# Performance work log

Measured on AMD Instinct MI355X. Metric: run time of the kernel, lower is better.

Reference implementation:

```python
import jax, jax.numpy as jnp
import numpy as np

KH, KW = 3, 3
STRIDE = (1, 1)
PAD = (1, 1)
DIL = (1, 1)

def _unfold(x, kh, kw, stride, padding, dilation):
    # Faithful torch.nn.functional.unfold: output (B, C*kh*kw, L) with
    # feature ordering channel-slowest, then kh, then kw.
    B, C, H, W = x.shape
    h_out = (H + 2 * padding[0] - dilation[0] * (kh - 1) - 1) // stride[0] + 1
    w_out = (W + 2 * padding[1] - dilation[1] * (kw - 1) - 1) // stride[1] + 1
    xp = jnp.pad(x, ((0, 0), (0, 0), (padding[0], padding[0]), (padding[1], padding[1])))
    rows = []
    for i in range(kh):  # small fixed kernel loop (9 slices), not a data-dim loop
        for j in range(kw):
            r0 = i * dilation[0]
            c0 = j * dilation[1]
            patch = xp[:, :, r0:r0 + h_out * stride[0]:stride[0],
                             c0:c0 + w_out * stride[1]:stride[1]]  # (B,C,h_out,w_out)
            rows.append(patch)
    # stack -> (B, C, kh*kw, h_out, w_out); reorder so feature dim = C*kh*kw
    p = jnp.stack(rows, axis=2)
    p = p.reshape(B, C * kh * kw, h_out * w_out)
    return p, h_out, w_out

def transform_transposed_unfolded_input(inp_unf):
    # Default hook: identity (as in the base class).
    return inp_unf

def reference(x, weight, bias):
    B = x.shape[0]
    O = weight.shape[0]
    inp_unf, h_out, w_out = _unfold(x, KH, KW, STRIDE, PAD, DIL)   # (B, C*k*k, L)
    inp_t = jnp.swapaxes(inp_unf, 1, 2)                            # (B, L, C*k*k)
    inp_t = transform_transposed_unfolded_input(inp_t)
    w2d = weight.reshape(O, -1)                                    # (O, C*k*k)
    out_unf = jnp.einsum('blk,ok->bol', inp_t, w2d)                # (B, O, L)
    out = out_unf.reshape(B, O, h_out, w_out)
    out = out + bias.reshape(1, O, 1, 1)
    return out

def setup_inputs() -> dict:
    key = jax.random.key(0)
    k1, k2, k3 = jax.random.split(key, 3)
    x = jax.random.normal(k1, (32, 128, 56, 56), dtype=jnp.float32)
    fan_in = 128 * KH * KW
    weight = jax.random.normal(k2, (256, 128, KH, KW), dtype=jnp.float32) / np.sqrt(fan_in)
    bias = jax.random.normal(k3, (256,), dtype=jnp.float32) * 0.01
    return {"x": x, "weight": weight, "bias": bias}
```

## Files before the change

### kernel.cpp

```cpp
#include <hip/hip_runtime.h>
#include <hip/hip_bf16.h>
#include <cstdint>

typedef float f32x4 __attribute__((ext_vector_type(4)));
typedef short bf16x8 __attribute__((ext_vector_type(8)));
typedef short short8 __attribute__((ext_vector_type(8)));

#define CIN   128
#define WIMG  56
#define HWSZ  3136
#define OCH   256
#define HP    58
#define WP    58

__global__ void small_prep(const float* __restrict__ wsrc,
                           __hip_bfloat16* __restrict__ wb,
                           __hip_bfloat16* __restrict__ xb) {
    int bidx = blockIdx.x;
    if (bidx < 456) {
        int idx = bidx * 256 + threadIdx.x;
        int c8  = idx & 15;
        int t   = idx >> 4;
        int b   = t / 228;
        int pos = t - b * 228;
        int h, w;
        if (pos < 58)       { h = 0;             w = pos; }
        else if (pos < 116) { h = 57;            w = pos - 58; }
        else if (pos < 172) { h = pos - 116 + 1; w = 0; }
        else                { h = pos - 172 + 1; w = 57; }
        uint4 z = {0, 0, 0, 0};
        *(uint4*)((char*)xb + (((size_t)(b * HP + h) * WP + w) * CIN + c8 * 8) * 2) = z;
    } else {
        int idx = (bidx - 456) * 256 + threadIdx.x;
        int c    = idx & 127;
        int rest = idx >> 7;
        int o    = rest & 255;
        int ij   = rest >> 8;
        wb[idx] = __float2bfloat16(wsrc[((size_t)o * CIN + c) * 9 + ij]);
    }
}

__global__ __launch_bounds__(256)
void cast_transpose_x(const float* __restrict__ x,
                      __hip_bfloat16* __restrict__ xb) {
    __shared__ float tile[64][33];
    const int hw0 = blockIdx.x * 32;
    const int c0  = blockIdx.y * 64;
    const int b   = blockIdx.z;

    const int lx = threadIdx.x & 31;
    const int lc = threadIdx.x >> 5;
    const float* src = x + ((size_t)(b * CIN + c0 + lc) * HWSZ) + hw0 + lx;
#pragma unroll
    for (int k = 0; k < 8; ++k)
        tile[lc + k * 8][lx] = src[(size_t)(k * 8) * HWSZ];
    __syncthreads();

    const int slot = threadIdx.x & 7;
    const int hwl  = threadIdx.x >> 3;
    int hw = hw0 + hwl;
    int h = hw / WIMG;
    int w = hw - h * WIMG;
    short8 v;
#pragma unroll
    for (int j = 0; j < 8; ++j) {
        __hip_bfloat16 hb = __float2bfloat16(tile[slot * 8 + j][hwl]);
        v[j] = *reinterpret_cast<short*>(&hb);
    }
    *(short8*)(xb + (((size_t)b * HP + (h + 1)) * WP + (w + 1)) * CIN + c0 + slot * 8) = v;
}

__device__ __forceinline__ void gload16(const void* g, void* l) {
    __builtin_amdgcn_global_load_lds(
        (const __attribute__((address_space(1))) unsigned*)g,
        (__attribute__((address_space(3))) unsigned*)l,
        16, 0, 0);
}

__global__ __launch_bounds__(512, 2)
void conv_gemm(const __hip_bfloat16* __restrict__ xb,
               const __hip_bfloat16* __restrict__ wb,
               const float* __restrict__ bias,
               float* __restrict__ out) {
    extern __shared__ __attribute__((aligned(16))) char smem[];

    const int tid = threadIdx.x;
    const int wv  = tid >> 6;
    const int ln  = tid & 63;

    int bid = blockIdx.x;
    bid = (bid & 7) * 49 + (bid >> 3);
    const int m0 = bid * 256;

    const int srow = tid >> 3;
    const int cs   = tid & 7;
    const int colsrc = ((cs * 16) ^ ((srow & 7) << 4)) >> 1;
    int aOff[4], bOff[4];
#pragma unroll
    for (int q = 0; q < 4; ++q) {
        int row = q * 64 + srow;
        int p  = m0 + row;
        int b  = p / HWSZ;
        int hw = p - b * HWSZ;
        int h  = hw / WIMG;
        int w  = hw - h * WIMG;
        aOff[q] = ((b * HP + h) * WP + w) * CIN + colsrc;
        bOff[q] = row * CIN + colsrc;
    }
    const int ldsd = tid * 16;

#define SA(buf,q,offA_) gload16(xb + aOff[q] + (offA_), smem + (buf)*65536 + (q)*8192 + ldsd)
#define SB(buf,q,offB_) gload16(wb + bOff[q] + (offB_), smem + (buf)*65536 + 32768 + (q)*8192 + ldsd)

    const int wm  = wv >> 2;
    const int wn  = wv & 3;
    const int fr  = ln & 15;
    const int kby = (ln >> 4) * 16;
    const int swz = (ln & 7) << 4;

    f32x4 acc[8][4] = {};
    bf16x8 af[4][2], bq0[2][2], bq1[2][2];

#define READ_A(base, mh) do {                                                 \
    _Pragma("unroll") for (int mi = 0; mi < 4; ++mi)                          \
    _Pragma("unroll") for (int kk = 0; kk < 2; ++kk)                          \
        af[mi][kk] = *(const bf16x8*)((base) +                                \
            (wm*128 + (mh)*64 + mi*16 + fr)*128 + ((kk*64 + kby) ^ swz));     \
} while (0)

#define READ_B(base, nh, dst) do {                                            \
    _Pragma("unroll") for (int ni = 0; ni < 2; ++ni)                          \
    _Pragma("unroll") for (int kk = 0; kk < 2; ++kk)                          \
        dst[ni][kk] = *(const bf16x8*)((base) + 32768 +                       \
            (wn*64 + (nh)*32 + ni*16 + fr)*128 + ((kk*64 + kby) ^ swz));      \
} while (0)

#define MQ(mh, nh, B) do {                                                    \
    _Pragma("unroll") for (int kk = 0; kk < 2; ++kk)                          \
    _Pragma("unroll") for (int mi = 0; mi < 4; ++mi)                          \
    _Pragma("unroll") for (int ni = 0; ni < 2; ++ni)                          \
        acc[(mh)*4+mi][(nh)*2+ni] = __builtin_amdgcn_mfma_f32_16x16x32_bf16(  \
            af[mi][kk], B[ni][kk], acc[(mh)*4+mi][(nh)*2+ni], 0, 0, 0);       \
} while (0)

#define VMW(N) do {                                                           \
    asm volatile("s_waitcnt vmcnt(" #N ")" ::: "memory");                     \
    __builtin_amdgcn_sched_barrier(0);                                        \
} while (0)

#define PHASE(MQCALL) do {                                                    \
    __builtin_amdgcn_s_barrier();                                             \
    asm volatile("s_waitcnt lgkmcnt(0)" ::: "memory");                        \
    __builtin_amdgcn_sched_barrier(0);                                        \
    __builtin_amdgcn_s_setprio(1);                                            \
    MQCALL;                                                                   \
    __builtin_amdgcn_s_setprio(0);                                            \
    __builtin_amdgcn_sched_barrier(0);                                        \
} while (0)

    const char* base0 = smem;
    const char* base1 = smem + 65536;

    SA(0,0,0); SA(0,2,0); SB(0,0,0); SB(0,1,0); SB(0,2,0); SB(0,3,0); SA(0,1,0); SA(0,3,0);
    SA(1,0,64); SA(1,2,64);
    asm volatile("s_waitcnt vmcnt(2)" ::: "memory");
    __builtin_amdgcn_s_barrier();

#pragma unroll 1
    for (int i = 0; i < 9; ++i) {
        const int iiA = i / 3,       jjA = i - 3 * iiA;
        const int iiB = (i + 1) / 3, jjB = (i + 1) - 3 * iiB;
        const int offA1 = (iiA * WP + jjA) * CIN + 64;
        const int offB1 = i * (OCH * CIN) + 64;
        const int offA2 = (iiB * WP + jjB) * CIN;
        const int offB2 = (i + 1) * (OCH * CIN);
        const int offA3 = offA2 + 64;
        const bool pf = (i < 8);

        READ_A(base0, 0);
        READ_B(base0, 0, bq0);
        SB(1,0,offB1); SB(1,1,offB1);
        PHASE(MQ(0, 0, bq0));
        __builtin_amdgcn_s_barrier();

        READ_B(base0, 1, bq1);
        SB(1,2,offB1); SB(1,3,offB1);
        PHASE(MQ(0, 1, bq1));
        VMW(6);
        __builtin_amdgcn_s_barrier();

        READ_A(base0, 1);
        SA(1,1,offA1); SA(1,3,offA1);
        PHASE(MQ(1, 1, bq1));
        __builtin_amdgcn_s_barrier();

        if (pf) { SA(0,0,offA2); SA(0,2,offA2); }
        PHASE(MQ(1, 0, bq0));
        if (pf) VMW(4); else VMW(2);
        __builtin_amdgcn_s_barrier();

        READ_A(base1, 0);
        READ_B(base1, 0, bq0);
        if (pf) { SB(0,0,offB2); SB(0,1,offB2); }
        PHASE(MQ(0, 0, bq0));
        __builtin_amdgcn_s_barrier();

        READ_B(base1, 1, bq1);
        if (pf) { SB(0,2,offB2); SB(0,3,offB2); }
        PHASE(MQ(0, 1, bq1));
        if (pf) VMW(6); else VMW(0);
        __builtin_amdgcn_s_barrier();

        READ_A(base1, 1);
        if (pf) { SA(0,1,offA2); SA(0,3,offA2); }
        PHASE(MQ(1, 1, bq1));
        __builtin_amdgcn_s_barrier();

        if (pf) { SA(1,0,offA3); SA(1,2,offA3); }
        PHASE(MQ(1, 0, bq0));
        if (pf) {
            VMW(4);
            __builtin_amdgcn_s_barrier();
        }
    }
#undef SA
#undef SB
#undef READ_A
#undef READ_B
#undef MQ
#undef PHASE
#undef VMW

    const int laneR4 = (ln >> 4) * 4;
    float bn[4];
#pragma unroll
    for (int ni = 0; ni < 4; ++ni)
        bn[ni] = bias[wn * 64 + ni * 16 + fr];

#pragma unroll
    for (int mi = 0; mi < 8; ++mi) {
        int p0 = m0 + wm * 128 + mi * 16 + laneR4;
        int b  = p0 / HWSZ;
        int hw = p0 - b * HWSZ;
#pragma unroll
        for (int ni = 0; ni < 4; ++ni) {
            int n = wn * 64 + ni * 16 + fr;
            float4 v;
            v.x = acc[mi][ni][0] + bn[ni];
            v.y = acc[mi][ni][1] + bn[ni];
            v.z = acc[mi][ni][2] + bn[ni];
            v.w = acc[mi][ni][3] + bn[ni];
            *(float4*)(out + ((size_t)(b * OCH + n) * HWSZ + hw)) = v;
        }
    }
}

extern "C" void kernel_launch(void* const* d_in, const int* in_sizes, int n_in,
                              void* d_out, int out_size, void* d_ws, size_t ws_size,
                              hipStream_t stream) {
    const float* x    = (const float*)d_in[0];
    const float* w    = (const float*)d_in[1];
    const float* bias = (const float*)d_in[2];
    float* out = (float*)d_out;

    char* ws = (char*)d_ws;
    __hip_bfloat16* xbuf = (__hip_bfloat16*)ws;
    __hip_bfloat16* wbuf = (__hip_bfloat16*)(ws + 27557888);

    hipFuncSetAttribute(reinterpret_cast<const void*>(conv_gemm),
                        hipFuncAttributeMaxDynamicSharedMemorySize, 131072);

    small_prep<<<1608, 256, 0, stream>>>(w, wbuf, xbuf);
    cast_transpose_x<<<dim3(98, 2, 32), dim3(256), 0, stream>>>(x, xbuf);
    conv_gemm<<<392, 512, 131072, stream>>>(xbuf, wbuf, bias, out);
}
```

Measured before the change: 100.5 us.

## Software-pipeline LDS fragment reads with double-buffered A/B registers in GEMM loop

Restructures the main K loop of the implicit-GEMM conv kernel so LDS-to-register fragment reads for the next MFMA quadrant are issued before and during the current quadrant's MFMAs. It uses separate A register sets (af0/af1) and even/odd B sets, with partial lgkmcnt waits replacing full waits. Global-to-LDS prefetch is regrouped so whole A+B half-tiles are issued together, and the prologue preloads the first fragments. This is meant to hide LDS read latency behind matrix math, at the cost of more VGPRs and a more delicate waitcnt and barrier ordering.

```diff
diff --git a/kernel.cpp b/kernel.cpp
--- a/kernel.cpp
+++ b/kernel.cpp
@@ -110,7 +110,7 @@
     const int ldsd = tid * 16;
 
 #define SA(buf,q,offA_) gload16(xb + aOff[q] + (offA_), smem + (buf)*65536 + (q)*8192 + ldsd)
-#define SB(buf,q,offB_) gload16(wb + bOff[q] + (offB_), smem + (buf)*65536 + 32768 + (q)*8192 + ldsd)
+#define SBW(buf,q,offB_) gload16(wb + bOff[q] + (offB_), smem + (buf)*65536 + 32768 + (q)*8192 + ldsd)
 
     const int wm  = wv >> 2;
     const int wn  = wv & 3;
@@ -119,117 +119,117 @@
     const int swz = (ln & 7) << 4;
 
     f32x4 acc[8][4] = {};
-    bf16x8 af[4][2], bq0[2][2], bq1[2][2];
-
-#define READ_A(base, mh) do {                                                 \
+    bf16x8 af0[4][2], af1[4][2], bq0E[2][2], bq0O[2][2], bq1[2][2];
+
+#define READ_AF(base, mh, dst) do {                                           \
     _Pragma("unroll") for (int mi = 0; mi < 4; ++mi)                          \
     _Pragma("unroll") for (int kk = 0; kk < 2; ++kk)                          \
-        af[mi][kk] = *(const bf16x8*)((base) +                                \
+        dst[mi][kk] = *(const bf16x8*)((base) +                               \
             (wm*128 + (mh)*64 + mi*16 + fr)*128 + ((kk*64 + kby) ^ swz));     \
 } while (0)
 
-#define READ_B(base, nh, dst) do {                                            \
+#define READ_BF(base, nh, dst) do {                                           \
     _Pragma("unroll") for (int ni = 0; ni < 2; ++ni)                          \
     _Pragma("unroll") for (int kk = 0; kk < 2; ++kk)                          \
         dst[ni][kk] = *(const bf16x8*)((base) + 32768 +                       \
             (wn*64 + (nh)*32 + ni*16 + fr)*128 + ((kk*64 + kby) ^ swz));      \
 } while (0)
 
-#define MQ(mh, nh, B) do {                                                    \
+#define MQ(mh, nh, A, B) do {                                                 \
     _Pragma("unroll") for (int kk = 0; kk < 2; ++kk)                          \
     _Pragma("unroll") for (int mi = 0; mi < 4; ++mi)                          \
     _Pragma("unroll") for (int ni = 0; ni < 2; ++ni)                          \
         acc[(mh)*4+mi][(nh)*2+ni] = __builtin_amdgcn_mfma_f32_16x16x32_bf16(  \
-            af[mi][kk], B[ni][kk], acc[(mh)*4+mi][(nh)*2+ni], 0, 0, 0);       \
+            A[mi][kk], B[ni][kk], acc[(mh)*4+mi][(nh)*2+ni], 0, 0, 0);        \
 } while (0)
 
-#define VMW(N) do {                                                           \
-    asm volatile("s_waitcnt vmcnt(" #N ")" ::: "memory");                     \
-    __builtin_amdgcn_sched_barrier(0);                                        \
-} while (0)
-
-#define PHASE(MQCALL) do {                                                    \
-    __builtin_amdgcn_s_barrier();                                             \
-    asm volatile("s_waitcnt lgkmcnt(0)" ::: "memory");                        \
-    __builtin_amdgcn_sched_barrier(0);                                        \
-    __builtin_amdgcn_s_setprio(1);                                            \
-    MQCALL;                                                                   \
-    __builtin_amdgcn_s_setprio(0);                                            \
-    __builtin_amdgcn_sched_barrier(0);                                        \
-} while (0)
+#define LGKM(N) do { asm volatile("s_waitcnt lgkmcnt(" #N ")" ::: "memory");  \
+                     __builtin_amdgcn_sched_barrier(0); } while (0)
+#define VMW(N)  do { asm volatile("s_waitcnt vmcnt(" #N ")" ::: "memory");    \
+                     __builtin_amdgcn_sched_barrier(0); } while (0)
+#define FEN     __builtin_amdgcn_sched_barrier(0)
+#define BAR     __builtin_amdgcn_s_barrier()
+#define PRIO_MQ(mh, nh, A, B) do { __builtin_amdgcn_s_setprio(1);             \
+    MQ(mh, nh, A, B); __builtin_amdgcn_s_setprio(0); FEN; } while (0)
 
     const char* base0 = smem;
     const char* base1 = smem + 65536;
 
-    SA(0,0,0); SA(0,2,0); SB(0,0,0); SB(0,1,0); SB(0,2,0); SB(0,3,0); SA(0,1,0); SA(0,3,0);
-    SA(1,0,64); SA(1,2,64);
-    asm volatile("s_waitcnt vmcnt(2)" ::: "memory");
-    __builtin_amdgcn_s_barrier();
+    SA(0,0,0); SA(0,2,0); SBW(0,0,0); SBW(0,1,0); SBW(0,2,0); SBW(0,3,0); SA(0,1,0); SA(0,3,0);
+    SA(1,0,64); SA(1,2,64); SBW(1,0,64); SBW(1,1,64); SBW(1,2,64); SBW(1,3,64);
+    VMW(6);
+    BAR;
+    READ_AF(base0, 0, af0); READ_BF(base0, 0, bq0E); READ_BF(base0, 1, bq1);
+    FEN;
 
 #pragma unroll 1
     for (int i = 0; i < 9; ++i) {
         const int iiA = i / 3,       jjA = i - 3 * iiA;
         const int iiB = (i + 1) / 3, jjB = (i + 1) - 3 * iiB;
-        const int offA1 = (iiA * WP + jjA) * CIN + 64;
-        const int offB1 = i * (OCH * CIN) + 64;
-        const int offA2 = (iiB * WP + jjB) * CIN;
-        const int offB2 = (i + 1) * (OCH * CIN);
-        const int offA3 = offA2 + 64;
+        const int offAO1 = (iiA * WP + jjA) * CIN + 64;
+        const int offAE2 = (iiB * WP + jjB) * CIN;
+        const int offBE2 = (i + 1) * (OCH * CIN);
+        const int offAO3 = offAE2 + 64;
+        const int offBO3 = offBE2 + 64;
         const bool pf = (i < 8);
 
-        READ_A(base0, 0);
-        READ_B(base0, 0, bq0);
-        SB(1,0,offB1); SB(1,1,offB1);
-        PHASE(MQ(0, 0, bq0));
-        __builtin_amdgcn_s_barrier();
-
-        READ_B(base0, 1, bq1);
-        SB(1,2,offB1); SB(1,3,offB1);
-        PHASE(MQ(0, 1, bq1));
-        VMW(6);
-        __builtin_amdgcn_s_barrier();
-
-        READ_A(base0, 1);
-        SA(1,1,offA1); SA(1,3,offA1);
-        PHASE(MQ(1, 1, bq1));
-        __builtin_amdgcn_s_barrier();
-
-        if (pf) { SA(0,0,offA2); SA(0,2,offA2); }
-        PHASE(MQ(1, 0, bq0));
-        if (pf) VMW(4); else VMW(2);
-        __builtin_amdgcn_s_barrier();
-
-        READ_A(base1, 0);
-        READ_B(base1, 0, bq0);
-        if (pf) { SB(0,0,offB2); SB(0,1,offB2); }
-        PHASE(MQ(0, 0, bq0));
-        __builtin_amdgcn_s_barrier();
-
-        READ_B(base1, 1, bq1);
-        if (pf) { SB(0,2,offB2); SB(0,3,offB2); }
-        PHASE(MQ(0, 1, bq1));
+        LGKM(4);
+        SA(1,1,offAO1); SA(1,3,offAO1); FEN;
+        PRIO_MQ(0, 0, af0, bq0E);
+        READ_AF(base0, 1, af1); FEN;
+        BAR;
+
+        LGKM(8);
+        PRIO_MQ(0, 1, af0, bq1);
+        VMW(2);
+        BAR;
+
+        LGKM(0);
+        PRIO_MQ(1, 1, af1, bq1);
+        READ_AF(base1, 0, af0); READ_BF(base1, 0, bq0O); READ_BF(base1, 1, bq1); FEN;
+        BAR;
+
+        if (pf) { SA(0,0,offAE2); SA(0,2,offAE2);
+                  SBW(0,0,offBE2); SBW(0,1,offBE2); SBW(0,2,offBE2); SBW(0,3,offBE2); }
+        FEN;
+        PRIO_MQ(1, 0, af1, bq0E);
         if (pf) VMW(6); else VMW(0);
-        __builtin_amdgcn_s_barrier();
-
-        READ_A(base1, 1);
-        if (pf) { SA(0,1,offA2); SA(0,3,offA2); }
-        PHASE(MQ(1, 1, bq1));
-        __builtin_amdgcn_s_barrier();
-
-        if (pf) { SA(1,0,offA3); SA(1,2,offA3); }
-        PHASE(MQ(1, 0, bq0));
-        if (pf) {
-            VMW(4);
-            __builtin_amdgcn_s_barrier();
-        }
+        BAR;
+
+        LGKM(4);
+        if (pf) { SA(0,1,offAE2); SA(0,3,offAE2); }
+        FEN;
+        PRIO_MQ(0, 0, af0, bq0O);
+        READ_AF(base1, 1, af1); FEN;
+        BAR;
+
+        LGKM(8);
+        PRIO_MQ(0, 1, af0, bq1);
+        if (pf) VMW(2);
+        BAR;
+
+        LGKM(0);
+        PRIO_MQ(1, 1, af1, bq1);
+        if (pf) { READ_AF(base0, 0, af0); READ_BF(base0, 0, bq0E); READ_BF(base0, 1, bq1); }
+        FEN;
+        BAR;
+
+        if (pf) { SA(1,0,offAO3); SA(1,2,offAO3);
+                  SBW(1,0,offBO3); SBW(1,1,offBO3); SBW(1,2,offBO3); SBW(1,3,offBO3); }
+        FEN;
+        PRIO_MQ(1, 0, af1, bq0O);
+        if (pf) { VMW(6); BAR; }
     }
 #undef SA
-#undef SB
-#undef READ_A
-#undef READ_B
+#undef SBW
+#undef READ_AF
+#undef READ_BF
 #undef MQ
-#undef PHASE
+#undef PRIO_MQ
+#undef LGKM
 #undef VMW
+#undef FEN
+#undef BAR
 
     const int laneR4 = (ln >> 4) * 4;
     float bn[4];
```

After: 225.6 us. +124.5%, slower.
